# Optimization experiments

Measured on AMD Instinct MI355X. Metric: run time of the kernel, lower is better.

The kernel has to match this reference:

```python
import jax, jax.numpy as jnp
import numpy as np

N_EMBD = 1024
N_HEAD = 16

def setup_inputs() -> dict:
    key = jax.random.key(0)
    ks = jax.random.split(key, 5)
    x = jax.random.normal(ks[0], (4, 2048, N_EMBD), dtype=jnp.float32)
    # torch Linear default init ~ U(-1/sqrt(fan_in), 1/sqrt(fan_in)); use scaled normals
    s = 1.0 / np.sqrt(N_EMBD)
    W_attn = jax.random.normal(ks[1], (N_EMBD, 3 * N_EMBD), dtype=jnp.float32) * s
    b_attn = jax.random.normal(ks[2], (3 * N_EMBD,), dtype=jnp.float32) * s
    W_proj = jax.random.normal(ks[3], (N_EMBD, N_EMBD), dtype=jnp.float32) * s
    b_proj = jax.random.normal(ks[4], (N_EMBD,), dtype=jnp.float32) * s
    return {"x": x, "W_attn": W_attn, "b_attn": b_attn, "W_proj": W_proj, "b_proj": b_proj}

def reference(x, W_attn, b_attn, W_proj, b_proj) -> jnp.ndarray:
    B, T, C = x.shape
    H = N_HEAD
    D = C // H  # head dim
    qkv = x @ W_attn + b_attn  # [B,T,3C]
    q, k, v = jnp.split(qkv, 3, axis=-1)
    # [B,T,C] -> [B,H,T,D]
    q = q.reshape(B, T, H, D).transpose(0, 2, 1, 3)
    k = k.reshape(B, T, H, D).transpose(0, 2, 1, 3)
    v = v.reshape(B, T, H, D).transpose(0, 2, 1, 3)
    scale = 1.0 / jnp.sqrt(jnp.float32(D))
    att = jnp.einsum('bhqd,bhkd->bhqk', q, k) * scale  # [B,H,T,T]
    causal = jnp.tril(jnp.ones((T, T), dtype=bool))
    att = jnp.where(causal[None, None, :, :], att, -jnp.inf)
    att = jax.nn.softmax(att, axis=-1)
    y = jnp.einsum('bhqk,bhkd->bhqd', att, v)  # [B,H,T,D]
    y = y.transpose(0, 2, 1, 3).reshape(B, T, C)
    return y @ W_proj + b_proj
```

## Files before the change

kernel.cpp:

```cpp
#include <hip/hip_runtime.h>
#include <stdint.h>


typedef __attribute__((ext_vector_type(8))) short short8;
typedef __attribute__((ext_vector_type(4))) float floatx4;

#define AS1C(p) ((const __attribute__((address_space(1))) void*)(p))
#define AS3(p)  ((__attribute__((address_space(3))) void*)(p))
#define GL16(src, dst) __builtin_amdgcn_global_load_lds(AS1C(src), AS3(dst), 16, 0, 0)

__device__ __forceinline__ unsigned short f2bf(float f) {
  unsigned int u = __builtin_bit_cast(unsigned int, f);
  u = (u + 0x7fffu + ((u >> 16) & 1u)) >> 16;
  return (unsigned short)u;
}
__device__ __forceinline__ unsigned short f2bf_trunc(float f) {
  return (unsigned short)(__builtin_bit_cast(unsigned int, f) >> 16);
}

__global__ void k_cvt(const float* __restrict__ in, unsigned short* __restrict__ out, int n4) {
  int i = blockIdx.x * blockDim.x + threadIdx.x;
  if (i < n4) {
    float4 v = ((const float4*)in)[i];
    ushort4 o;
    o.x = f2bf(v.x); o.y = f2bf(v.y); o.z = f2bf(v.z); o.w = f2bf(v.w);
    ((ushort4*)out)[i] = o;
  }
}

__global__ void k_tw(const float* __restrict__ in, unsigned short* __restrict__ out, int K, int N) {
  __shared__ float t[32][33];
  int n0 = blockIdx.x * 32, k0 = blockIdx.y * 32;
  int tx = threadIdx.x, ty = threadIdx.y;
#pragma unroll
  for (int i = 0; i < 4; i++)
    t[ty + 8 * i][tx] = in[(size_t)(k0 + ty + 8 * i) * N + n0 + tx];
  __syncthreads();
#pragma unroll
  for (int i = 0; i < 4; i++)
    out[(size_t)(n0 + ty + 8 * i) * K + k0 + tx] = f2bf(t[tx][ty + 8 * i]);
}

__global__ void k_tv(const unsigned short* __restrict__ qkv, unsigned short* __restrict__ vt) {
  __shared__ unsigned short t[32][33];
  int t0 = blockIdx.x * 32;
  int d0 = blockIdx.y * 32;
  int bh = blockIdx.z;
  int b = bh >> 4, h = bh & 15;
  int tx = threadIdx.x, ty = threadIdx.y;
#pragma unroll
  for (int i = 0; i < 4; i++)
    t[ty + 8 * i][tx] = qkv[(size_t)(b * 2048 + t0 + ty + 8 * i) * 3072 + 2048 + h * 64 + d0 + tx];
  __syncthreads();
#pragma unroll
  for (int i = 0; i < 4; i++)
    vt[(size_t)(bh * 64 + d0 + ty + 8 * i) * 2048 + t0 + tx] = t[tx][ty + 8 * i];
}

template <int OUT_F32>
__global__ __launch_bounds__(512, 2)
void k_gemm8(const unsigned short* __restrict__ A,
             const unsigned short* __restrict__ Bt,
             const float* __restrict__ bias,
             void* __restrict__ Cout, int M, int N, int K) {
  __shared__ unsigned short lA[2][256 * 64];
  __shared__ unsigned short lB[2][128 * 64];
  int tid = threadIdx.x;
  int lane = tid & 63, wv = tid >> 6;
  int lc = lane & 15, quad = lane >> 4;
  int sw = lc & 7;

  unsigned nbx = gridDim.x;
  unsigned nwg = nbx * gridDim.y;
  unsigned flat = blockIdx.y * nbx + blockIdx.x;
  unsigned cpx = nwg >> 3;
  unsigned tile = (flat & 7u) * cpx + (flat >> 3);
  int n0 = (int)(tile % nbx) * 128;
  int m0 = (int)(tile / nbx) * 256;

  int wm = (wv >> 1) * 64;
  int wn = (wv & 1) * 64;

  floatx4 acc[4][4];
#pragma unroll
  for (int i = 0; i < 4; i++)
#pragma unroll
    for (int j = 0; j < 4; j++) acc[i][j] = (floatx4){0.f, 0.f, 0.f, 0.f};

  int srow = tid >> 3;
  int scol = ((tid & 7) ^ (srow & 7)) * 8;
  const unsigned short* gA = A + (size_t)(m0 + srow) * K + scol;
  const unsigned short* gB = Bt + (size_t)(n0 + srow) * K + scol;

  int NT = K >> 6;

#pragma unroll
  for (int i = 0; i < 4; i++)
    GL16(gA + (size_t)(i * 64) * K, &lA[0][i * 4096 + wv * 512]);
#pragma unroll
  for (int i = 0; i < 2; i++)
    GL16(gB + (size_t)(i * 64) * K, &lB[0][i * 4096 + wv * 512]);

  for (int t = 0; t < NT; t++) {
    const unsigned short* bufA = lA[t & 1];
    const unsigned short* bufB = lB[t & 1];

    if (t + 1 < NT) {
      unsigned short* nA = lA[(t + 1) & 1];
      unsigned short* nB = lB[(t + 1) & 1];
      int k0 = (t + 1) << 6;
#pragma unroll
      for (int i = 0; i < 4; i++)
        GL16(gA + (size_t)(i * 64) * K + k0, nA + i * 4096 + wv * 512);
#pragma unroll
      for (int i = 0; i < 2; i++)
        GL16(gB + (size_t)(i * 64) * K + k0, nB + i * 4096 + wv * 512);
      asm volatile("s_waitcnt vmcnt(6)" ::: "memory");
    } else {
      asm volatile("s_waitcnt vmcnt(0)" ::: "memory");
    }
    __builtin_amdgcn_s_barrier();
    asm volatile("" ::: "memory");

    short8 af[4][2];
#pragma unroll
    for (int m = 0; m < 4; m++)
#pragma unroll
      for (int ks = 0; ks < 2; ks++)
        af[m][ks] = *(const short8*)(bufA + (wm + m * 16 + lc) * 64 + (((ks * 4 + quad) ^ sw) * 8));
    short8 bf0[2][2];
#pragma unroll
    for (int n = 0; n < 2; n++)
#pragma unroll
      for (int ks = 0; ks < 2; ks++)
        bf0[n][ks] = *(const short8*)(bufB + (wn + n * 16 + lc) * 64 + (((ks * 4 + quad) ^ sw) * 8));
    __builtin_amdgcn_s_setprio(1);
#pragma unroll
    for (int m = 0; m < 4; m++)
#pragma unroll
      for (int n = 0; n < 2; n++)
#pragma unroll
        for (int ks = 0; ks < 2; ks++)
          acc[m][n] = __builtin_amdgcn_mfma_f32_16x16x32_bf16(af[m][ks], bf0[n][ks], acc[m][n], 0, 0, 0);
    __builtin_amdgcn_s_setprio(0);
    asm volatile("" ::: "memory");
    __builtin_amdgcn_s_barrier();
    asm volatile("" ::: "memory");

    short8 bf1[2][2];
#pragma unroll
    for (int n = 0; n < 2; n++)
#pragma unroll
      for (int ks = 0; ks < 2; ks++)
        bf1[n][ks] = *(const short8*)(bufB + (wn + (n + 2) * 16 + lc) * 64 + (((ks * 4 + quad) ^ sw) * 8));
    __builtin_amdgcn_s_setprio(1);
#pragma unroll
    for (int m = 0; m < 4; m++)
#pragma unroll
      for (int n = 0; n < 2; n++)
#pragma unroll
        for (int ks = 0; ks < 2; ks++)
          acc[m][n + 2] = __builtin_amdgcn_mfma_f32_16x16x32_bf16(af[m][ks], bf1[n][ks], acc[m][n + 2], 0, 0, 0);
    __builtin_amdgcn_s_setprio(0);
    asm volatile("" ::: "memory");
    __builtin_amdgcn_s_barrier();
    asm volatile("" ::: "memory");
  }

  float bv[4];
#pragma unroll
  for (int j = 0; j < 4; j++) bv[j] = bias[n0 + wn + j * 16 + lc];
#pragma unroll
  for (int i = 0; i < 4; i++) {
#pragma unroll
    for (int j = 0; j < 4; j++) {
#pragma unroll
      for (int r = 0; r < 4; r++) {
        size_t idx = (size_t)(m0 + wm + i * 16 + quad * 4 + r) * N + (n0 + wn + j * 16 + lc);
        float v = acc[i][j][r] + bv[j];
        if (OUT_F32) ((float*)Cout)[idx] = v;
        else         ((unsigned short*)Cout)[idx] = f2bf(v);
      }
    }
  }
}

#define LP_STRIDE 68
__global__ __launch_bounds__(256, 4)
void k_flash(const unsigned short* __restrict__ qkv,
             const unsigned short* __restrict__ vt,
             unsigned short* __restrict__ y) {
  __shared__ unsigned short lK[64 * 64];
  __shared__ unsigned short lVT[64 * 64];
  __shared__ unsigned short lP[4][2][16 * LP_STRIDE];
  int tid = threadIdx.x, lane = tid & 63, wv = tid >> 6;
  int lc = lane & 15, quad = lane >> 4;
  int sw = lc & 7;
  int j  = blockIdx.x;
  int bh = blockIdx.y;
  int b = bh >> 4, h = bh & 15;
  int qtA = j, qtB = 31 - j;
  int qrA = qtA * 64 + wv * 16;
  int qrB = qtB * 64 + wv * 16;

  short8 qfA[2], qfB[2];
  {
    const unsigned short* qp = qkv + (size_t)(b * 2048 + qrA + lc) * 3072 + h * 64 + quad * 8;
    qfA[0] = *(const short8*)qp;
    qfA[1] = *(const short8*)(qp + 32);
  }
  {
    const unsigned short* qp = qkv + (size_t)(b * 2048 + qrB + lc) * 3072 + h * 64 + quad * 8;
    qfB[0] = *(const short8*)qp;
    qfB[1] = *(const short8*)(qp + 32);
  }

  float rsA[4] = {0.f, 0.f, 0.f, 0.f}, rsB[4] = {0.f, 0.f, 0.f, 0.f};
  floatx4 oA[4], oB[4];
#pragma unroll
  for (int dt = 0; dt < 4; dt++) {
    oA[dt] = (floatx4){0.f, 0.f, 0.f, 0.f};
    oB[dt] = (floatx4){0.f, 0.f, 0.f, 0.f};
  }

  int srow = tid >> 3;
  int scol = ((tid & 7) ^ (srow & 7)) * 8;
  const unsigned short* gK = qkv + (size_t)(b * 2048 + srow) * 3072 + 1024 + h * 64 + scol;
  const unsigned short* gV = vt + (size_t)(bh * 64 + srow) * 2048 + scol;

  const float SC2 = 0.18033688011f;
  int nt = qtB + 1;

  for (int kv = 0; kv < nt; kv++) {
    int kv0 = kv * 64;
#pragma unroll
    for (int c = 0; c < 2; c++) {
      __builtin_amdgcn_global_load_lds(AS1C(gK + (size_t)(kv0 + 32 * c) * 3072),
                                       AS3(lK + (32 * c + 8 * wv) * 64), 16, 0, 0);
      __builtin_amdgcn_global_load_lds(AS1C(gV + (size_t)(32 * c) * 2048 + kv0),
                                       AS3(lVT + (32 * c + 8 * wv) * 64), 16, 0, 0);
    }
    __syncthreads();

    bool withA = (kv <= qtA);

    floatx4 sB[4], sA[4];
#pragma unroll
    for (int n = 0; n < 4; n++) {
      short8 kf0 = *(const short8*)(lK + (n * 16 + lc) * 64 + ((quad ^ sw) * 8));
      short8 kf1 = *(const short8*)(lK + (n * 16 + lc) * 64 + (((4 + quad) ^ sw) * 8));
      floatx4 t = (floatx4){0.f, 0.f, 0.f, 0.f};
      t = __builtin_amdgcn_mfma_f32_16x16x32_bf16(qfB[0], kf0, t, 0, 0, 0);
      t = __builtin_amdgcn_mfma_f32_16x16x32_bf16(qfB[1], kf1, t, 0, 0, 0);
      sB[n] = t;
      if (withA) {
        floatx4 u = (floatx4){0.f, 0.f, 0.f, 0.f};
        u = __builtin_amdgcn_mfma_f32_16x16x32_bf16(qfA[0], kf0, u, 0, 0, 0);
        u = __builtin_amdgcn_mfma_f32_16x16x32_bf16(qfA[1], kf1, u, 0, 0, 0);
        sA[n] = u;
      }
    }

    {
      bool diag = (kv == qtB);
#pragma unroll
      for (int n = 0; n < 4; n++)
#pragma unroll
        for (int r = 0; r < 4; r++) {
          float arg = sB[n][r] * SC2;
          if (diag && (kv0 + n * 16 + lc > qrB + quad * 4 + r)) arg = -__builtin_inff();
          float p = __builtin_amdgcn_exp2f(arg);
          rsB[r] += p;
          lP[wv][0][(quad * 4 + r) * LP_STRIDE + n * 16 + lc] = f2bf_trunc(p);
        }
    }
    if (withA) {
      bool diag = (kv == qtA);
#pragma unroll
      for (int n = 0; n < 4; n++)
#pragma unroll
        for (int r = 0; r < 4; r++) {
          float arg = sA[n][r] * SC2;
          if (diag && (kv0 + n * 16 + lc > qrA + quad * 4 + r)) arg = -__builtin_inff();
          float p = __builtin_amdgcn_exp2f(arg);
          rsA[r] += p;
          lP[wv][1][(quad * 4 + r) * LP_STRIDE + n * 16 + lc] = f2bf_trunc(p);
        }
    }

#pragma unroll
    for (int s2 = 0; s2 < 2; s2++) {
      short8 pfB = *(const short8*)(&lP[wv][0][0] + lc * LP_STRIDE + s2 * 32 + quad * 8);
      short8 pfA;
      if (withA) pfA = *(const short8*)(&lP[wv][1][0] + lc * LP_STRIDE + s2 * 32 + quad * 8);
#pragma unroll
      for (int dt = 0; dt < 4; dt++) {
        short8 vf = *(const short8*)(lVT + (dt * 16 + lc) * 64 + (((s2 * 4 + quad) ^ sw) * 8));
        oB[dt] = __builtin_amdgcn_mfma_f32_16x16x32_bf16(pfB, vf, oB[dt], 0, 0, 0);
        if (withA) oA[dt] = __builtin_amdgcn_mfma_f32_16x16x32_bf16(pfA, vf, oA[dt], 0, 0, 0);
      }
    }
    __syncthreads();
  }

#pragma unroll
  for (int off = 1; off < 16; off <<= 1)
#pragma unroll
    for (int r = 0; r < 4; r++) {
      rsA[r] += __shfl_xor(rsA[r], off);
      rsB[r] += __shfl_xor(rsB[r], off);
    }
#pragma unroll
  for (int r = 0; r < 4; r++) {
    float invA = 1.0f / rsA[r];
    float invB = 1.0f / rsB[r];
#pragma unroll
    for (int dt = 0; dt < 4; dt++) {
      size_t ia = (size_t)(b * 2048 + qrA + quad * 4 + r) * 1024 + h * 64 + dt * 16 + lc;
      size_t ib = (size_t)(b * 2048 + qrB + quad * 4 + r) * 1024 + h * 64 + dt * 16 + lc;
      y[ia] = f2bf(oA[dt][r] * invA);
      y[ib] = f2bf(oB[dt][r] * invB);
    }
  }
}

extern "C" void kernel_launch(void* const* d_in, const int* in_sizes, int n_in,
                              void* d_out, int out_size, void* d_ws, size_t ws_size,
                              hipStream_t stream) {
  const float* x      = (const float*)d_in[0];
  const float* W_attn = (const float*)d_in[1];
  const float* b_attn = (const float*)d_in[2];
  const float* W_proj = (const float*)d_in[3];
  const float* b_proj = (const float*)d_in[4];

  char* ws = (char*)d_ws;
  unsigned short* xb     = (unsigned short*)ws;
  unsigned short* wattnT = (unsigned short*)(ws + 16777216);
  unsigned short* wprojT = (unsigned short*)(ws + 23068672);
  unsigned short* qkv    = (unsigned short*)(ws + 25165824);
  unsigned short* vt     = (unsigned short*)(ws + 75497472);
  unsigned short* y      = xb;

  k_cvt<<<8192, 256, 0, stream>>>(x, xb, 8388608 / 4);
  k_tw<<<dim3(96, 32), dim3(32, 8), 0, stream>>>(W_attn, wattnT, 1024, 3072);
  k_tw<<<dim3(32, 32), dim3(32, 8), 0, stream>>>(W_proj, wprojT, 1024, 1024);
  k_gemm8<0><<<dim3(24, 32), 512, 0, stream>>>(xb, wattnT, b_attn, qkv, 8192, 3072, 1024);
  k_tv<<<dim3(64, 2, 64), dim3(32, 8), 0, stream>>>(qkv, vt);
  k_flash<<<dim3(16, 64), 256, 0, stream>>>(qkv, vt, y);
  k_gemm8<1><<<dim3(8, 32), 512, 0, stream>>>(y, wprojT, b_proj, d_out, 8192, 1024, 1024);
}
```

Measured before the change: 280.9 us.

## Enlarge GEMM tile to 256x256 with two-stage-ahead prefetch schedule

The bf16 GEMM tile grows from 256x128 to 256x256, and each wave now computes a 128x64 sub-tile with 32 accumulators. The loads for iteration t+2 are issued into the buffer just consumed, interleaved between MFMA phases, with a deeper vmcnt wait. This is meant to raise arithmetic intensity and hide global latency. In exchange it doubles LDS use and register pressure, and it halves the number of workgroups, which leaves the 1024-wide projection GEMM with only 128 blocks.

```diff
diff --git a/kernel.cpp b/kernel.cpp
--- a/kernel.cpp
+++ b/kernel.cpp
@@ -8,6 +8,7 @@
 #define AS1C(p) ((const __attribute__((address_space(1))) void*)(p))
 #define AS3(p)  ((__attribute__((address_space(3))) void*)(p))
 #define GL16(src, dst) __builtin_amdgcn_global_load_lds(AS1C(src), AS3(dst), 16, 0, 0)
+#define BARRIER() do { asm volatile("" ::: "memory"); __builtin_amdgcn_s_barrier(); asm volatile("" ::: "memory"); } while (0)
 
 __device__ __forceinline__ unsigned short f2bf(float f) {
   unsigned int u = __builtin_bit_cast(unsigned int, f);
@@ -64,7 +65,7 @@
              const float* __restrict__ bias,
              void* __restrict__ Cout, int M, int N, int K) {
   __shared__ unsigned short lA[2][256 * 64];
-  __shared__ unsigned short lB[2][128 * 64];
+  __shared__ unsigned short lB[2][256 * 64];
   int tid = threadIdx.x;
   int lane = tid & 63, wv = tid >> 6;
   int lc = lane & 15, quad = lane >> 4;
@@ -75,15 +76,15 @@
   unsigned flat = blockIdx.y * nbx + blockIdx.x;
   unsigned cpx = nwg >> 3;
   unsigned tile = (flat & 7u) * cpx + (flat >> 3);
-  int n0 = (int)(tile % nbx) * 128;
+  int n0 = (int)(tile % nbx) * 256;
   int m0 = (int)(tile / nbx) * 256;
 
-  int wm = (wv >> 1) * 64;
-  int wn = (wv & 1) * 64;
-
-  floatx4 acc[4][4];
-#pragma unroll
-  for (int i = 0; i < 4; i++)
+  int wm = (wv >> 2) * 128;
+  int wn = (wv & 3) * 64;
+
+  floatx4 acc[8][4];
+#pragma unroll
+  for (int i = 0; i < 8; i++)
 #pragma unroll
     for (int j = 0; j < 4; j++) acc[i][j] = (floatx4){0.f, 0.f, 0.f, 0.f};
 
@@ -95,45 +96,38 @@
   int NT = K >> 6;
 
 #pragma unroll
-  for (int i = 0; i < 4; i++)
-    GL16(gA + (size_t)(i * 64) * K, &lA[0][i * 4096 + wv * 512]);
-#pragma unroll
-  for (int i = 0; i < 2; i++)
-    GL16(gB + (size_t)(i * 64) * K, &lB[0][i * 4096 + wv * 512]);
-
-  for (int t = 0; t < NT; t++) {
+  for (int i = 0; i < 4; i++) GL16(gA + (size_t)(i * 64) * K, &lA[0][i * 4096 + wv * 512]);
+#pragma unroll
+  for (int i = 0; i < 4; i++) GL16(gB + (size_t)(i * 64) * K, &lB[0][i * 4096 + wv * 512]);
+#pragma unroll
+  for (int i = 0; i < 4; i++) GL16(gA + (size_t)(i * 64) * K + 64, &lA[1][i * 4096 + wv * 512]);
+#pragma unroll
+  for (int i = 0; i < 4; i++) GL16(gB + (size_t)(i * 64) * K + 64, &lB[1][i * 4096 + wv * 512]);
+  asm volatile("s_waitcnt vmcnt(8)" ::: "memory");
+  __builtin_amdgcn_s_barrier();
+  asm volatile("" ::: "memory");
+
+  for (int t = 0; t < NT; ++t) {
     const unsigned short* bufA = lA[t & 1];
     const unsigned short* bufB = lB[t & 1];
-
-    if (t + 1 < NT) {
-      unsigned short* nA = lA[(t + 1) & 1];
-      unsigned short* nB = lB[(t + 1) & 1];
-      int k0 = (t + 1) << 6;
-#pragma unroll
-      for (int i = 0; i < 4; i++)
-        GL16(gA + (size_t)(i * 64) * K + k0, nA + i * 4096 + wv * 512);
-#pragma unroll
-      for (int i = 0; i < 2; i++)
-        GL16(gB + (size_t)(i * 64) * K + k0, nB + i * 4096 + wv * 512);
-      asm volatile("s_waitcnt vmcnt(6)" ::: "memory");
-    } else {
-      asm volatile("s_waitcnt vmcnt(0)" ::: "memory");
-    }
-    __builtin_amdgcn_s_barrier();
-    asm volatile("" ::: "memory");
-
-    short8 af[4][2];
+    unsigned short* stA = lA[t & 1];
+    unsigned short* stB = lB[t & 1];
+    int k2 = (t + 2) << 6;
+    bool st = (t + 2) < NT;
+
+    short8 af[4][2], bf[4][2];
+
 #pragma unroll
     for (int m = 0; m < 4; m++)
 #pragma unroll
       for (int ks = 0; ks < 2; ks++)
         af[m][ks] = *(const short8*)(bufA + (wm + m * 16 + lc) * 64 + (((ks * 4 + quad) ^ sw) * 8));
-    short8 bf0[2][2];
 #pragma unroll
     for (int n = 0; n < 2; n++)
 #pragma unroll
       for (int ks = 0; ks < 2; ks++)
-        bf0[n][ks] = *(const short8*)(bufB + (wn + n * 16 + lc) * 64 + (((ks * 4 + quad) ^ sw) * 8));
+        bf[n][ks] = *(const short8*)(bufB + (wn + n * 16 + lc) * 64 + (((ks * 4 + quad) ^ sw) * 8));
+    BARRIER();
     __builtin_amdgcn_s_setprio(1);
 #pragma unroll
     for (int m = 0; m < 4; m++)
@@ -141,18 +135,16 @@
       for (int n = 0; n < 2; n++)
 #pragma unroll
         for (int ks = 0; ks < 2; ks++)
-          acc[m][n] = __builtin_amdgcn_mfma_f32_16x16x32_bf16(af[m][ks], bf0[n][ks], acc[m][n], 0, 0, 0);
+          acc[m][n] = __builtin_amdgcn_mfma_f32_16x16x32_bf16(af[m][ks], bf[n][ks], acc[m][n], 0, 0, 0);
     __builtin_amdgcn_s_setprio(0);
-    asm volatile("" ::: "memory");
-    __builtin_amdgcn_s_barrier();
-    asm volatile("" ::: "memory");
-
-    short8 bf1[2][2];
-#pragma unroll
-    for (int n = 0; n < 2; n++)
+    BARRIER();
+
+#pragma unroll
+    for (int n = 2; n < 4; n++)
 #pragma unroll
       for (int ks = 0; ks < 2; ks++)
-        bf1[n][ks] = *(const short8*)(bufB + (wn + (n + 2) * 16 + lc) * 64 + (((ks * 4 + quad) ^ sw) * 8));
+        bf[n][ks] = *(const short8*)(bufB + (wn + n * 16 + lc) * 64 + (((ks * 4 + quad) ^ sw) * 8));
+    BARRIER();
     __builtin_amdgcn_s_setprio(1);
 #pragma unroll
     for (int m = 0; m < 4; m++)
@@ -160,18 +152,56 @@
       for (int n = 0; n < 2; n++)
 #pragma unroll
         for (int ks = 0; ks < 2; ks++)
-          acc[m][n + 2] = __builtin_amdgcn_mfma_f32_16x16x32_bf16(af[m][ks], bf1[n][ks], acc[m][n + 2], 0, 0, 0);
+          acc[m][n + 2] = __builtin_amdgcn_mfma_f32_16x16x32_bf16(af[m][ks], bf[n + 2][ks], acc[m][n + 2], 0, 0, 0);
     __builtin_amdgcn_s_setprio(0);
-    asm volatile("" ::: "memory");
-    __builtin_amdgcn_s_barrier();
-    asm volatile("" ::: "memory");
+    BARRIER();
+
+#pragma unroll
+    for (int m = 0; m < 4; m++)
+#pragma unroll
+      for (int ks = 0; ks < 2; ks++)
+        af[m][ks] = *(const short8*)(bufA + (wm + (m + 4) * 16 + lc) * 64 + (((ks * 4 + quad) ^ sw) * 8));
+    if (st) {
+#pragma unroll
+      for (int i = 0; i < 4; i++)
+        GL16(gB + (size_t)(i * 64) * K + k2, stB + i * 4096 + wv * 512);
+    }
+    BARRIER();
+    __builtin_amdgcn_s_setprio(1);
+#pragma unroll
+    for (int m = 0; m < 4; m++)
+#pragma unroll
+      for (int n = 0; n < 2; n++)
+#pragma unroll
+        for (int ks = 0; ks < 2; ks++)
+          acc[m + 4][n] = __builtin_amdgcn_mfma_f32_16x16x32_bf16(af[m][ks], bf[n][ks], acc[m + 4][n], 0, 0, 0);
+    __builtin_amdgcn_s_setprio(0);
+    BARRIER();
+
+    if (st) {
+#pragma unroll
+      for (int i = 0; i < 4; i++)
+        GL16(gA + (size_t)(i * 64) * K + k2, stA + i * 4096 + wv * 512);
+    }
+    __builtin_amdgcn_s_setprio(1);
+#pragma unroll
+    for (int m = 0; m < 4; m++)
+#pragma unroll
+      for (int n = 0; n < 2; n++)
+#pragma unroll
+        for (int ks = 0; ks < 2; ks++)
+          acc[m + 4][n + 2] = __builtin_amdgcn_mfma_f32_16x16x32_bf16(af[m][ks], bf[n + 2][ks], acc[m + 4][n + 2], 0, 0, 0);
+    __builtin_amdgcn_s_setprio(0);
+    if (st) asm volatile("s_waitcnt vmcnt(8)" ::: "memory");
+    else    asm volatile("s_waitcnt vmcnt(0)" ::: "memory");
+    BARRIER();
   }
 
   float bv[4];
 #pragma unroll
   for (int j = 0; j < 4; j++) bv[j] = bias[n0 + wn + j * 16 + lc];
 #pragma unroll
-  for (int i = 0; i < 4; i++) {
+  for (int i = 0; i < 8; i++) {
 #pragma unroll
     for (int j = 0; j < 4; j++) {
 #pragma unroll
@@ -344,8 +374,8 @@
   k_cvt<<<8192, 256, 0, stream>>>(x, xb, 8388608 / 4);
   k_tw<<<dim3(96, 32), dim3(32, 8), 0, stream>>>(W_attn, wattnT, 1024, 3072);
   k_tw<<<dim3(32, 32), dim3(32, 8), 0, stream>>>(W_proj, wprojT, 1024, 1024);
-  k_gemm8<0><<<dim3(24, 32), 512, 0, stream>>>(xb, wattnT, b_attn, qkv, 8192, 3072, 1024);
+  k_gemm8<0><<<dim3(12, 32), 512, 0, stream>>>(xb, wattnT, b_attn, qkv, 8192, 3072, 1024);
   k_tv<<<dim3(64, 2, 64), dim3(32, 8), 0, stream>>>(qkv, vt);
   k_flash<<<dim3(16, 64), 256, 0, stream>>>(qkv, vt, y);
-  k_gemm8<1><<<dim3(8, 32), 512, 0, stream>>>(y, wprojT, b_proj, d_out, 8192, 1024, 1024);
-}
+  k_gemm8<1><<<dim3(4, 32), 512, 0, stream>>>(y, wprojT, b_proj, d_out, 8192, 1024, 1024);
+}
```

Measured after the change: 281.2 us. About the same (+0.1%).
